# Kernel optimization log

Measured on AMD Instinct MI355X. Metric: run time of the kernel, lower is better.

Reference implementation:

```python
import jax, jax.numpy as jnp
import numpy as np

N = 50000      # num nodes
E = 800000     # num edges (avg degree 16)
F_IN = 64      # num_node_features
D = 64         # layer_hidden_dim (= out_channels per layer)
H = 8          # num_heads
C = D // H     # head_dim = 8
L = 5          # num_gnn_layers


def setup_inputs() -> dict:
    key = jax.random.key(0)
    ks = jax.random.split(key, 8)
    x = jax.random.normal(ks[0], (N, F_IN), jnp.float32)
    edge_index = jax.random.randint(ks[1], (2, E), 0, N, dtype=jnp.int32)
    # input embedding Linear(F_IN, D): weight stored as [in, out]
    W_in = jax.random.normal(ks[2], (F_IN, D), jnp.float32) * 0.1
    b_in = jnp.zeros((D,), jnp.float32)
    # per-layer GAT params, stacked over L layers
    lin_w = jax.random.normal(ks[3], (L, D, D), jnp.float32) * 0.1
    lin_b = jnp.zeros((L, D), jnp.float32)
    att = jax.random.normal(ks[4], (L, H, 2 * C), jnp.float32) * 0.1
    out_bias = jnp.zeros((L, D), jnp.float32)
    ln_g = jnp.ones((L, D), jnp.float32)
    ln_b = jnp.zeros((L, D), jnp.float32)
    return {"x": x, "edge_index": edge_index, "W_in": W_in, "b_in": b_in,
            "lin_w": lin_w, "lin_b": lin_b, "att": att, "out_bias": out_bias,
            "ln_g": ln_g, "ln_b": ln_b}


def _gat_layer(h, src, dst, Wl, bl, al, ob, g, b):
    # h: [N, D] -> per-head features [N, H, C]
    hp = (h @ Wl + bl).reshape(N, H, C)
    xi = hp[dst]          # [E, H, C] target-node features (x_i)
    xj = hp[src]          # [E, H, C] source-node features (x_j)
    # cat([x_i, x_j]) . att  == x_i . att[:, :C] + x_j . att[:, C:]
    alpha = jnp.einsum('ehc,hc->eh', xi, al[:, :C]) + \
            jnp.einsum('ehc,hc->eh', xj, al[:, C:])          # [E, H]
    alpha = jax.nn.leaky_relu(alpha, negative_slope=0.2)
    # segment softmax over target index (numerically stable)
    m = jax.ops.segment_max(alpha, dst, num_segments=N)      # [N, H]
    ea = jnp.exp(alpha - m[dst])
    s = jax.ops.segment_sum(ea, dst, num_segments=N)         # [N, H]
    w = ea / (s[dst] + 1e-16)                                # [E, H]
    # message = x_j * alpha, aggr='add'
    agg = jax.ops.segment_sum(xj * w[:, :, None], dst, num_segments=N)  # [N, H, C]
    out = agg.reshape(N, H * C) + ob
    out = jax.nn.elu(out)
    # LayerNorm over feature dim (eval mode: dropout = identity)
    mu = out.mean(-1, keepdims=True)
    var = out.var(-1, keepdims=True)
    return (out - mu) * jax.lax.rsqrt(var + 1e-5) * g + b


def reference(x, edge_index, W_in, b_in, lin_w, lin_b, att, out_bias, ln_g, ln_b):
    src = edge_index[0]
    dst = edge_index[1]   # PyG source_to_target: index = edge_index[1]
    h = jax.nn.relu(x @ W_in + b_in)
    for l in range(L):
        h = _gat_layer(h, src, dst, lin_w[l], lin_b[l], att[l],
                       out_bias[l], ln_g[l], ln_b[l])
    return h
```

## Files before the change

### kernel.cpp

```cpp
#include <hip/hip_runtime.h>
#include <hip/hip_bf16.h>

#define DD 64
#define LL 5
#define KPAD 64
#define L2E 1.4426950408889634f

typedef __attribute__((ext_vector_type(8))) short short8;
typedef __attribute__((ext_vector_type(4))) float float4v;

__device__ __forceinline__ short f2bf_bits(float f) {
    __hip_bfloat16 h = __float2bfloat16(f);
    return *reinterpret_cast<short*>(&h);
}
__device__ __forceinline__ float bfbits2f(short s) {
    __hip_bfloat16 h = *reinterpret_cast<__hip_bfloat16*>(&s);
    return __bfloat162float(h);
}

__device__ __forceinline__ int sniffw(const unsigned short* xb) {
    int lane = threadIdx.x & 63;
    int e = (xb[lane * 2] >> 7) & 0xFF;
    return __any(e >= 134) ? 1 : 0;
}

__global__ void allcvt_k(const void* __restrict__ x, const void* __restrict__ W_in,
                         const void* __restrict__ b_in, const void* __restrict__ lw,
                         const void* __restrict__ lb, const void* __restrict__ att,
                         const void* __restrict__ ob, const void* __restrict__ lg,
                         const void* __restrict__ lbb,
                         float* __restrict__ wts,
                         unsigned short* __restrict__ whiT, unsigned short* __restrict__ wloT,
                         int* __restrict__ deg, int n) {
    int bid = blockIdx.x;
    int fl = sniffw((const unsigned short*)x);
    if (bid < 104) {
        int i = bid * 256 + threadIdx.x;
        if (i >= 26560) return;
        const void* p; int o;
        if      (i < 4096)  { p = W_in; o = i; }
        else if (i < 4160)  { p = b_in; o = i - 4096; }
        else if (i < 24640) { p = lw;   o = i - 4160; }
        else if (i < 24960) { p = lb;   o = i - 24640; }
        else if (i < 25600) { p = att;  o = i - 24960; }
        else if (i < 25920) { p = ob;   o = i - 25600; }
        else if (i < 26240) { p = lg;   o = i - 25920; }
        else                { p = lbb;  o = i - 26240; }
        wts[i] = fl ? ((const float*)p)[o] : (float)((const __hip_bfloat16*)p)[o];
    } else if (bid < 104 + 96) {
        int i = (bid - 104) * 256 + threadIdx.x;
        if (i >= 6 * 4096) return;
        const void* p; int o;
        if (i < 4096) { p = W_in; o = i; } else { p = lw; o = i - 4096; }
        float v = fl ? ((const float*)p)[o] : (float)((const __hip_bfloat16*)p)[o];
        short hi = f2bf_bits(v);
        short lo = f2bf_bits(v - bfbits2f(hi));
        int mat = i >> 12, rem = i & 4095, k = rem >> 6, col = rem & 63;
        int t = mat * 4096 + col * 64 + k;
        whiT[t] = (unsigned short)hi;
        wloT[t] = (unsigned short)lo;
    } else {
        int i = (bid - 104 - 96) * 256 + threadIdx.x;
        if (i < n) deg[i] = 0;
    }
}

__device__ __forceinline__ void gemm_from_lds(
        const unsigned short (*AH)[72], const unsigned short (*AL)[72],
        const unsigned short* __restrict__ Whi, const unsigned short* __restrict__ Wlo,
        const float* __restrict__ bias, const float* __restrict__ Att,
        unsigned short* __restrict__ hp_out, float* __restrict__ bd,
        float* __restrict__ ss, int base, int n) {
    int lane = threadIdx.x & 63;
    int wave = threadIdx.x >> 6;
    int m = lane & 15;
    int q = lane >> 4;
    int coln = wave * 16 + m;

    short8 ah0 = *reinterpret_cast<const short8*>(&AH[m][q * 8]);
    short8 ah1 = *reinterpret_cast<const short8*>(&AH[m][32 + q * 8]);
    short8 al0 = *reinterpret_cast<const short8*>(&AL[m][q * 8]);
    short8 al1 = *reinterpret_cast<const short8*>(&AL[m][32 + q * 8]);

    short8 bh0 = *reinterpret_cast<const short8*>(Whi + coln * 64 + q * 8);
    short8 bh1 = *reinterpret_cast<const short8*>(Whi + coln * 64 + 32 + q * 8);
    short8 bl0 = *reinterpret_cast<const short8*>(Wlo + coln * 64 + q * 8);
    short8 bl1 = *reinterpret_cast<const short8*>(Wlo + coln * 64 + 32 + q * 8);

    float4v acc = {0.f, 0.f, 0.f, 0.f};
    acc = __builtin_amdgcn_mfma_f32_16x16x32_bf16(ah0, bh0, acc, 0, 0, 0);
    acc = __builtin_amdgcn_mfma_f32_16x16x32_bf16(al0, bh0, acc, 0, 0, 0);
    acc = __builtin_amdgcn_mfma_f32_16x16x32_bf16(ah0, bl0, acc, 0, 0, 0);
    acc = __builtin_amdgcn_mfma_f32_16x16x32_bf16(ah1, bh1, acc, 0, 0, 0);
    acc = __builtin_amdgcn_mfma_f32_16x16x32_bf16(al1, bh1, acc, 0, 0, 0);
    acc = __builtin_amdgcn_mfma_f32_16x16x32_bf16(ah1, bl1, acc, 0, 0, 0);

    float bc = bias[coln];
    int c_ = m & 7;
    int hh = 2 * wave + (m >> 3);
    float attd = Att[hh * 16 + c_];
    float atts = Att[hh * 16 + 8 + c_];
#pragma unroll
    for (int r = 0; r < 4; ++r) {
        int rr = base + q * 4 + r;
        float v = acc[r] + bc;
        short vb = f2bf_bits(v);
        float vr = bfbits2f(vb);
        if (rr < n) hp_out[(size_t)rr * 64 + coln] = (unsigned short)vb;
        float bdv = vr * attd;
        float ssv = vr * atts;
        bdv += __shfl_xor(bdv, 1, 64);
        bdv += __shfl_xor(bdv, 2, 64);
        bdv += __shfl_xor(bdv, 4, 64);
        ssv += __shfl_xor(ssv, 1, 64);
        ssv += __shfl_xor(ssv, 2, 64);
        ssv += __shfl_xor(ssv, 4, 64);
        if ((m & 7) == 0 && rr < n) {
            bd[rr * 8 + hh] = bdv * L2E;
            ss[rr * 8 + hh] = ssv * L2E;
        }
    }
}

__global__ void __launch_bounds__(256) k0c_k(const void* __restrict__ x,
                                             const int* __restrict__ src,
                                             const int* __restrict__ dst,
                                             int* __restrict__ deg,
                                             unsigned short* __restrict__ csr_pad,
                                             const unsigned short* __restrict__ whiT,
                                             const unsigned short* __restrict__ wloT,
                                             const float* __restrict__ bias_in,
                                             const float* __restrict__ bias_l0,
                                             const float* __restrict__ att0,
                                             unsigned short* __restrict__ hp_out,
                                             float* __restrict__ bd, float* __restrict__ ss,
                                             int n, int e, int psize, int chunks, int nbk) {
    __shared__ unsigned short AH[16][72];
    __shared__ unsigned short AL[16][72];
    int bid = blockIdx.x;
    int grp = bid >> 3;
    int sub = bid & 7;

    if ((grp & 1) == 0) {
        int chunk = grp >> 1;
        if (chunk < chunks) {
            int p = sub;
            int lo = p * psize;
            int hi = min(lo + psize, n);
            int ebase = chunk * 2048 + threadIdx.x;
#pragma unroll
            for (int k = 0; k < 8; ++k) {
                int i = ebase + k * 256;
                if (i < e) {
                    int d = dst[i];
                    if (d >= lo && d < hi) {
                        int slot = atomicAdd(&deg[d], 1);
                        if (slot < KPAD) csr_pad[d * KPAD + slot] = (unsigned short)src[i];
                    }
                }
            }
        }
        return;
    }

    int kb = (grp >> 1) * 8 + sub;
    if (kb >= nbk) return;
    int lane = threadIdx.x & 63;
    int wave = threadIdx.x >> 6;
    int m = lane & 15;
    int q = lane >> 4;
    int coln = wave * 16 + m;
    int base = kb * 16;

    int fl = sniffw((const unsigned short*)x);

    {
        int arow = min(base + m, n - 1);
        short8 ah0, ah1, al0, al1;
        if (fl) {
            const float* xr = (const float*)x + (size_t)arow * 64;
            const float4* p0 = reinterpret_cast<const float4*>(xr + q * 8);
            const float4* p1 = reinterpret_cast<const float4*>(xr + 32 + q * 8);
            float4 f00 = p0[0], f01 = p0[1];
            float4 f10 = p1[0], f11 = p1[1];
            float fs0[8] = {f00.x, f00.y, f00.z, f00.w, f01.x, f01.y, f01.z, f01.w};
            float fs1[8] = {f10.x, f10.y, f10.z, f10.w, f11.x, f11.y, f11.z, f11.w};
#pragma unroll
            for (int k = 0; k < 8; ++k) {
                short h0 = f2bf_bits(fs0[k]);
                ah0[k] = h0;
                al0[k] = f2bf_bits(fs0[k] - bfbits2f(h0));
                short h1 = f2bf_bits(fs1[k]);
                ah1[k] = h1;
                al1[k] = f2bf_bits(fs1[k] - bfbits2f(h1));
            }
        } else {
            const unsigned short* xr = (const unsigned short*)x + (size_t)arow * 64;
            ah0 = *reinterpret_cast<const short8*>(xr + q * 8);
            ah1 = *reinterpret_cast<const short8*>(xr + 32 + q * 8);
            short8 z = {0, 0, 0, 0, 0, 0, 0, 0};
            al0 = z;
            al1 = z;
        }
        short8 bh0 = *reinterpret_cast<const short8*>(whiT + coln * 64 + q * 8);
        short8 bh1 = *reinterpret_cast<const short8*>(whiT + coln * 64 + 32 + q * 8);
        short8 bl0 = *reinterpret_cast<const short8*>(wloT + coln * 64 + q * 8);
        short8 bl1 = *reinterpret_cast<const short8*>(wloT + coln * 64 + 32 + q * 8);
        float4v acc = {0.f, 0.f, 0.f, 0.f};
        acc = __builtin_amdgcn_mfma_f32_16x16x32_bf16(ah0, bh0, acc, 0, 0, 0);
        acc = __builtin_amdgcn_mfma_f32_16x16x32_bf16(al0, bh0, acc, 0, 0, 0);
        acc = __builtin_amdgcn_mfma_f32_16x16x32_bf16(ah0, bl0, acc, 0, 0, 0);
        acc = __builtin_amdgcn_mfma_f32_16x16x32_bf16(ah1, bh1, acc, 0, 0, 0);
        acc = __builtin_amdgcn_mfma_f32_16x16x32_bf16(al1, bh1, acc, 0, 0, 0);
        acc = __builtin_amdgcn_mfma_f32_16x16x32_bf16(ah1, bl1, acc, 0, 0, 0);
        float bc = bias_in[coln];
#pragma unroll
        for (int r = 0; r < 4; ++r) {
            float v = fmaxf(acc[r] + bc, 0.f);
            short hi = f2bf_bits(v);
            AH[q * 4 + r][coln] = (unsigned short)hi;
            AL[q * 4 + r][coln] = (unsigned short)f2bf_bits(v - bfbits2f(hi));
        }
    }
    __syncthreads();
    gemm_from_lds(AH, AL, whiT + 4096, wloT + 4096, bias_l0, att0,
                  hp_out, bd, ss, base, n);
}

#define EXJ(W, j) { unsigned ws_ = (e1 & 4) ? ((e1 & 2) ? W.w : W.z) : ((e1 & 2) ? W.y : W.x); \
    j = (e1 & 1) ? (int)(ws_ >> 16) : (int)(ws_ & 0xffffu); j = min(j, nm1); }
#define EXG(W, g0, g1) { unsigned d0_ = (qt & 2) ? W.y : W.x; unsigned d1_ = (qt & 2) ? W.w : W.z; \
    g0 = (qt & 1) ? (int)(d0_ >> 16) : (int)(d0_ & 0xffffu); \
    g1 = (qt & 1) ? (int)(d1_ >> 16) : (int)(d1_ & 0xffffu); \
    g0 = min(g0, nm1); g1 = min(g1, nm1); }
#define FMA4(V, W, A0, A1, A2, A3) \
    A0 = fmaf(__int_as_float((int)(V.x << 16)), W, A0); \
    A1 = fmaf(__int_as_float((int)(V.x & 0xffff0000u)), W, A1); \
    A2 = fmaf(__int_as_float((int)(V.y << 16)), W, A2); \
    A3 = fmaf(__int_as_float((int)(V.y & 0xffff0000u)), W, A3);

#define ISSUE(c, WA, WB) \
    int jA_##c; EXJ(WA, jA_##c) \
    int jB_##c; EXJ(WB, jB_##c) \
    float ssA_##c = ss_in[jA_##c * 8 + h1]; \
    float ssB_##c = ss_in[jB_##c * 8 + h1]; \
    int gA0_##c; int gA1_##c; EXG(WA, gA0_##c, gA1_##c) \
    int gB0_##c; int gB1_##c; EXG(WB, gB0_##c, gB1_##c) \
    uint2 vA0_##c = *reinterpret_cast<const uint2*>(hpbf + (size_t)gA0_##c * 64 + fq4); \
    uint2 vA1_##c = *reinterpret_cast<const uint2*>(hpbf + (size_t)gA1_##c * 64 + fq4); \
    uint2 vB0_##c = *reinterpret_cast<const uint2*>(hpbf + (size_t)gB0_##c * 64 + fq4); \
    uint2 vB1_##c = *reinterpret_cast<const uint2*>(hpbf + (size_t)gB1_##c * 64 + fq4);

#define COMP(c) { \
    int slot_ = c * 8 + e1; \
    if (c < ncA) { \
        float aa_ = bhA + ssA_##c; aa_ = (aa_ > 0.f) ? aa_ : 0.2f * aa_; \
        float wg_ = (slot_ < ddA) ? exp2f(fminf(aa_, 60.f)) : 0.f; \
        sA += wg_; \
        float w0_ = __int_as_float(__builtin_amdgcn_ds_bpermute(bb, __float_as_int(wg_))); \
        float w1_ = __int_as_float(__builtin_amdgcn_ds_bpermute(bb + 128, __float_as_int(wg_))); \
        FMA4(vA0_##c, w0_, aA0, aA1, aA2, aA3) \
        FMA4(vA1_##c, w1_, aA0, aA1, aA2, aA3) \
    } \
    if (c < ncB) { \
        float aa_ = bhB + ssB_##c; aa_ = (aa_ > 0.f) ? aa_ : 0.2f * aa_; \
        float wg_ = (slot_ < ddB) ? exp2f(fminf(aa_, 60.f)) : 0.f; \
        sB += wg_; \
        float w0_ = __int_as_float(__builtin_amdgcn_ds_bpermute(bb, __float_as_int(wg_))); \
        float w1_ = __int_as_float(__builtin_amdgcn_ds_bpermute(bb + 128, __float_as_int(wg_))); \
        FMA4(vB0_##c, w0_, aB0, aB1, aB2, aB3) \
        FMA4(vB1_##c, w1_, aB0, aB1, aB2, aB3) \
    } }

__device__ __forceinline__ void gat_half(
        const unsigned short* __restrict__ hpbf,
        const float* __restrict__ ss_in,
        const unsigned short* __restrict__ csr,
        int uA, int uB, int ddA, int ddB, float bhA, float bhB,
        int e1, int h1, int qt, int fq4, int bb, int nm1,
        int qselA, int qselB,
        float& r0, float& r1, float& r2, float& r3, float& rsum) {
    const uint4* cA = reinterpret_cast<const uint4*>(csr + (size_t)uA * KPAD);
    const uint4* cB = reinterpret_cast<const uint4*>(csr + (size_t)uB * KPAD);
    uint4 wa0 = cA[0], wa1 = cA[1], wa2 = cA[2], wa3 = cA[3];
    uint4 wb0 = cB[0], wb1 = cB[1], wb2 = cB[2], wb3 = cB[3];
    int ncA = (ddA + 7) >> 3;
    int ncB = (ddB + 7) >> 3;
    int ncm = max(ncA, ncB);

    float sA = 0.f, sB = 0.f;
    float aA0 = 0.f, aA1 = 0.f, aA2 = 0.f, aA3 = 0.f;
    float aB0 = 0.f, aB1 = 0.f, aB2 = 0.f, aB3 = 0.f;

    if (ncm <= 2) {
        ISSUE(0, wa0, wb0)
        ISSUE(1, wa1, wb1)
        COMP(0)
        COMP(1)
    } else if (ncm == 3) {
        ISSUE(0, wa0, wb0)
        ISSUE(1, wa1, wb1)
        COMP(0)
        ISSUE(2, wa2, wb2)
        COMP(1)
        COMP(2)
    } else {
        ISSUE(0, wa0, wb0)
        ISSUE(1, wa1, wb1)
        COMP(0)
        ISSUE(2, wa2, wb2)
        COMP(1)
        ISSUE(3, wa3, wb3)
        COMP(2)
        COMP(3)
        for (int c = 4; c < ncm; ++c) {
            uint4 wac = cA[c];
            uint4 wbc = cB[c];
            int jA; EXJ(wac, jA)
            int jB; EXJ(wbc, jB)
            float ssAv = ss_in[jA * 8 + h1];
            float ssBv = ss_in[jB * 8 + h1];
            int gA0; int gA1; EXG(wac, gA0, gA1)
            int gB0; int gB1; EXG(wbc, gB0, gB1)
            uint2 vA0 = *reinterpret_cast<const uint2*>(hpbf + (size_t)gA0 * 64 + fq4);
            uint2 vA1 = *reinterpret_cast<const uint2*>(hpbf + (size_t)gA1 * 64 + fq4);
            uint2 vB0 = *reinterpret_cast<const uint2*>(hpbf + (size_t)gB0 * 64 + fq4);
            uint2 vB1 = *reinterpret_cast<const uint2*>(hpbf + (size_t)gB1 * 64 + fq4);
            int slot_ = c * 8 + e1;
            if (c < ncA) {
                float aa_ = bhA + ssAv; aa_ = (aa_ > 0.f) ? aa_ : 0.2f * aa_;
                float wg_ = (slot_ < ddA) ? exp2f(fminf(aa_, 60.f)) : 0.f;
                sA += wg_;
                float w0_ = __int_as_float(__builtin_amdgcn_ds_bpermute(bb, __float_as_int(wg_)));
                float w1_ = __int_as_float(__builtin_amdgcn_ds_bpermute(bb + 128, __float_as_int(wg_)));
                FMA4(vA0, w0_, aA0, aA1, aA2, aA3)
                FMA4(vA1, w1_, aA0, aA1, aA2, aA3)
            }
            if (c < ncB) {
                float aa_ = bhB + ssBv; aa_ = (aa_ > 0.f) ? aa_ : 0.2f * aa_;
                float wg_ = (slot_ < ddB) ? exp2f(fminf(aa_, 60.f)) : 0.f;
                sB += wg_;
                float w0_ = __int_as_float(__builtin_amdgcn_ds_bpermute(bb, __float_as_int(wg_)));
                float w1_ = __int_as_float(__builtin_amdgcn_ds_bpermute(bb + 128, __float_as_int(wg_)));
                FMA4(vB0, w0_, aB0, aB1, aB2, aB3)
                FMA4(vB1, w1_, aB0, aB1, aB2, aB3)
            }
        }
    }

    float ssumA = sA;
    ssumA += __shfl_xor(ssumA, 8, 64);
    ssumA += __shfl_xor(ssumA, 16, 64);
    ssumA += __shfl_xor(ssumA, 32, 64);
    float ssumB = sB;
    ssumB += __shfl_xor(ssumB, 8, 64);
    ssumB += __shfl_xor(ssumB, 16, 64);
    ssumB += __shfl_xor(ssumB, 32, 64);

    aA0 += __shfl_xor(aA0, 16, 64); aA0 += __shfl_xor(aA0, 32, 64);
    aA1 += __shfl_xor(aA1, 16, 64); aA1 += __shfl_xor(aA1, 32, 64);
    aA2 += __shfl_xor(aA2, 16, 64); aA2 += __shfl_xor(aA2, 32, 64);
    aA3 += __shfl_xor(aA3, 16, 64); aA3 += __shfl_xor(aA3, 32, 64);
    aB0 += __shfl_xor(aB0, 16, 64); aB0 += __shfl_xor(aB0, 32, 64);
    aB1 += __shfl_xor(aB1, 16, 64); aB1 += __shfl_xor(aB1, 32, 64);
    aB2 += __shfl_xor(aB2, 16, 64); aB2 += __shfl_xor(aB2, 32, 64);
    aB3 += __shfl_xor(aB3, 16, 64); aB3 += __shfl_xor(aB3, 32, 64);

    if (qt == qselA) { r0 = aA0; r1 = aA1; r2 = aA2; r3 = aA3; rsum = ssumA; }
    if (qt == qselB) { r0 = aB0; r1 = aB1; r2 = aB2; r3 = aB3; rsum = ssumB; }
}

__global__ void __launch_bounds__(256) layer_k(const unsigned short* __restrict__ hpbf,
                                               const int* __restrict__ deg,
                                               const unsigned short* __restrict__ csr,
                                               const float* __restrict__ bd_in,
                                               const float* __restrict__ ss_in,
                                               const float* __restrict__ ob,
                                               const float* __restrict__ g,
                                               const float* __restrict__ b,
                                               const unsigned short* __restrict__ Wnhi,
                                               const unsigned short* __restrict__ Wnlo,
                                               const float* __restrict__ bias_n,
                                               const float* __restrict__ att_n,
                                               unsigned short* __restrict__ hp_out,
                                               float* __restrict__ bd_out,
                                               float* __restrict__ ss_out,
                                               void* __restrict__ outp,
                                               const unsigned short* __restrict__ xb,
                                               int n, int last) {
    __shared__ unsigned short AH[16][72];
    __shared__ unsigned short AL[16][72];
    int lane = threadIdx.x & 63;
    int wave = threadIdx.x >> 6;
    int base = blockIdx.x * 16;

    int h1 = lane & 7;
    int e1 = lane >> 3;
    int qt = lane >> 4;
    int fq = lane & 15;
    int fq4 = fq * 4;
    int h2 = fq >> 1;
    int bb = qt * 32 + h2 * 4;
    int nm1 = n - 1;

    int fl = last ? sniffw(xb) : 0;

    int nd0 = base + wave * 4;
    int4 dv = *reinterpret_cast<const int4*>(deg + nd0);
    int dd0 = __builtin_amdgcn_readfirstlane((nd0 + 0 < n) ? min(dv.x, KPAD) : 0);
    int dd1 = __builtin_amdgcn_readfirstlane((nd0 + 1 < n) ? min(dv.y, KPAD) : 0);
    int dd2 = __builtin_amdgcn_readfirstlane((nd0 + 2 < n) ? min(dv.z, KPAD) : 0);
    int dd3 = __builtin_amdgcn_readfirstlane((nd0 + 3 < n) ? min(dv.w, KPAD) : 0);
    float bhv0 = bd_in[min(nd0 + 0, nm1) * 8 + h1];
    float bhv1 = bd_in[min(nd0 + 1, nm1) * 8 + h1];
    float bhv2 = bd_in[min(nd0 + 2, nm1) * 8 + h1];
    float bhv3 = bd_in[min(nd0 + 3, nm1) * 8 + h1];
    int u0 = __builtin_amdgcn_readfirstlane(min(nd0 + 0, nm1));
    int u1 = __builtin_amdgcn_readfirstlane(min(nd0 + 1, nm1));
    int u2 = __builtin_amdgcn_readfirstlane(min(nd0 + 2, nm1));
    int u3 = __builtin_amdgcn_readfirstlane(min(nd0 + 3, nm1));

    float r0 = 0.f, r1 = 0.f, r2 = 0.f, r3 = 0.f, rsum = 0.f;

    gat_half(hpbf, ss_in, csr, u0, u1, dd0, dd1, bhv0, bhv1,
             e1, h1, qt, fq4, bb, nm1, 0, 1, r0, r1, r2, r3, rsum);
    gat_half(hpbf, ss_in, csr, u2, u3, dd2, dd3, bhv2, bhv3,
             e1, h1, qt, fq4, bb, nm1, 2, 3, r0, r1, r2, r3, rsum);

    float sh = __int_as_float(
        __builtin_amdgcn_ds_bpermute((qt * 16 + h2) * 4, __float_as_int(rsum)));
    float rinv = __builtin_amdgcn_rcpf(sh + 1e-16f);
    float4 ob4 = ((const float4*)ob)[fq];
    float o0 = r0 * rinv + ob4.x;
    float o1 = r1 * rinv + ob4.y;
    float o2 = r2 * rinv + ob4.z;
    float o3 = r3 * rinv + ob4.w;
    o0 = (o0 > 0.f) ? o0 : exp2f(o0 * L2E) - 1.f;
    o1 = (o1 > 0.f) ? o1 : exp2f(o1 * L2E) - 1.f;
    o2 = (o2 > 0.f) ? o2 : exp2f(o2 * L2E) - 1.f;
    o3 = (o3 > 0.f) ? o3 : exp2f(o3 * L2E) - 1.f;

    float ps = o0 + o1 + o2 + o3;
#pragma unroll
    for (int d = 1; d < 16; d <<= 1) ps += __shfl_xor(ps, d, 64);
    float mu = ps * (1.f / 64.f);
    float d0 = o0 - mu, d1 = o1 - mu, d2v = o2 - mu, d3 = o3 - mu;
    float sq = d0 * d0 + d1 * d1 + d2v * d2v + d3 * d3;
#pragma unroll
    for (int d = 1; d < 16; d <<= 1) sq += __shfl_xor(sq, d, 64);
    float rstd = __builtin_amdgcn_rsqf(sq * (1.f / 64.f) + 1e-5f);
    float4 g4 = ((const float4*)g)[fq];
    float4 b4 = ((const float4*)b)[fq];
    float y0 = d0 * rstd * g4.x + b4.x;
    float y1 = d1 * rstd * g4.y + b4.y;
    float y2 = d2v * rstd * g4.z + b4.z;
    float y3 = d3 * rstd * g4.w + b4.w;

    int onode = nd0 + qt;
    if (!last) {
        int ridx = wave * 4 + qt;
        short hb0 = f2bf_bits(y0), hb1 = f2bf_bits(y1);
        short hb2 = f2bf_bits(y2), hb3 = f2bf_bits(y3);
        unsigned hA = (unsigned short)hb0 | ((unsigned)(unsigned short)hb1 << 16);
        unsigned hB = (unsigned short)hb2 | ((unsigned)(unsigned short)hb3 << 16);
        uint2 yh = {hA, hB};
        unsigned lA = (unsigned short)f2bf_bits(y0 - bfbits2f(hb0)) |
                      ((unsigned)(unsigned short)f2bf_bits(y1 - bfbits2f(hb1)) << 16);
        unsigned lB = (unsigned short)f2bf_bits(y2 - bfbits2f(hb2)) |
                      ((unsigned)(unsigned short)f2bf_bits(y3 - bfbits2f(hb3)) << 16);
        uint2 yl = {lA, lB};
        *reinterpret_cast<uint2*>(&AH[ridx][fq * 4]) = yh;
        *reinterpret_cast<uint2*>(&AL[ridx][fq * 4]) = yl;
    } else if (onode < n) {
        if (fl) {
            float4 y = {y0, y1, y2, y3};
            ((float4*)outp)[(size_t)onode * 16 + fq] = y;
        } else {
            unsigned lo = (unsigned short)f2bf_bits(y0) |
                          ((unsigned)(unsigned short)f2bf_bits(y1) << 16);
            unsigned hi = (unsigned short)f2bf_bits(y2) |
                          ((unsigned)(unsigned short)f2bf_bits(y3) << 16);
            uint2 y = {lo, hi};
            ((uint2*)outp)[(size_t)onode * 16 + fq] = y;
        }
    }

    if (last) return;
    __syncthreads();
    gemm_from_lds(AH, AL, Wnhi, Wnlo, bias_n, att_n, hp_out, bd_out, ss_out, base, n);
}

static void* g_pool = nullptr;
static size_t g_pool_sz = 0;

extern "C" void kernel_launch(void* const* d_in, const int* in_sizes, int n_in,
                              void* d_out, int out_size, void* d_ws, size_t ws_size,
                              hipStream_t stream) {
    const void* x    = d_in[0];
    const int* ei    = (const int*)d_in[1];
    const void* W_in = d_in[2];
    const void* b_in = d_in[3];
    const void* lw   = d_in[4];
    const void* lb   = d_in[5];
    const void* att  = d_in[6];
    const void* ob   = d_in[7];
    const void* lg   = d_in[8];
    const void* lbb  = d_in[9];

    const int n = in_sizes[0] / DD;
    const int e = in_sizes[1] / 2;
    const int* src = ei;
    const int* dst = ei + e;

    auto align256 = [](size_t v) { return (v + 255) & ~(size_t)255; };
    size_t need = 0;
    size_t off_hpA  = need; need += align256((size_t)(n + 32) * DD * 2);
    size_t off_hpB  = need; need += align256((size_t)(n + 32) * DD * 2);
    size_t off_deg  = need; need += align256((size_t)(n + 32) * 4);
    size_t off_csr  = need; need += align256((size_t)n * KPAD * 2);
    size_t off_wts  = need; need += align256((size_t)26560 * 4);
    size_t off_bdA  = need; need += align256((size_t)n * 8 * 4);
    size_t off_ssA  = need; need += align256((size_t)n * 8 * 4);
    size_t off_bdB  = need; need += align256((size_t)n * 8 * 4);
    size_t off_ssB  = need; need += align256((size_t)n * 8 * 4);
    size_t off_whi  = need; need += align256((size_t)6 * 4096 * 2);
    size_t off_wlo  = need; need += align256((size_t)6 * 4096 * 2);

    char* ws;
    if (ws_size >= need) {
        ws = (char*)d_ws;
    } else {
        if (g_pool == nullptr || g_pool_sz < need) {
            hipMalloc(&g_pool, need);
            g_pool_sz = need;
        }
        ws = (char*)g_pool;
    }

    unsigned short* hpA = (unsigned short*)(ws + off_hpA);
    unsigned short* hpB = (unsigned short*)(ws + off_hpB);
    int* deg     = (int*)(ws + off_deg);
    unsigned short* csr = (unsigned short*)(ws + off_csr);
    float* wts   = (float*)(ws + off_wts);
    float* bdA   = (float*)(ws + off_bdA);
    float* ssA   = (float*)(ws + off_ssA);
    float* bdB   = (float*)(ws + off_bdB);
    float* ssB   = (float*)(ws + off_ssB);
    unsigned short* whiT = (unsigned short*)(ws + off_whi);
    unsigned short* wloT = (unsigned short*)(ws + off_wlo);

    float* wb_in = wts + 4096;
    float* wlb   = wts + 24640;
    float* watt  = wts + 24960;
    float* wob   = wts + 25600;
    float* wlg   = wts + 25920;
    float* wlbb  = wts + 26240;

    int degb = (n + 255) / 256;
    allcvt_k<<<104 + 96 + degb, 256, 0, stream>>>(
        x, W_in, b_in, lw, lb, att, ob, lg, lbb,
        wts, whiT, wloT, deg, n);

    int psize = (n + 7) / 8;
    int chunks = (e + 2047) / 2048;
    int nb16 = (n + 15) / 16;
    int k0g = (nb16 + 7) / 8;
    int ngrp = 2 * max(chunks, k0g);
    k0c_k<<<ngrp * 8, 256, 0, stream>>>(
        x, src, dst, deg, csr, whiT, wloT, wb_in, wlb, watt,
        hpA, bdA, ssA, n, e, psize, chunks, nb16);

    for (int l = 0; l < LL; ++l) {
        int last = (l == LL - 1) ? 1 : 0;
        unsigned short* hin = (l & 1) ? hpB : hpA;
        float* bdi = (l & 1) ? bdB : bdA;
        float* ssi = (l & 1) ? ssB : ssA;
        unsigned short* hout = (l & 1) ? hpA : hpB;
        float* bdo = (l & 1) ? bdA : bdB;
        float* sso = (l & 1) ? ssA : ssB;
        layer_k<<<nb16, 256, 0, stream>>>(
            hin, deg, csr, bdi, ssi,
            wob + (size_t)l * DD, wlg + (size_t)l * DD, wlbb + (size_t)l * DD,
            whiT + (size_t)(l + 2) * 4096, wloT + (size_t)(l + 2) * 4096,
            wlb + (size_t)(l + 1) * DD, watt + (size_t)(l + 1) * 128,
            hout, bdo, sso, d_out, (const unsigned short*)x, n, last);
    }
}
```

Before: 268.4 us.

## Fuse CSR build and all GAT layers into one persistent cooperative kernel

```diff
diff --git a/kernel.cpp b/kernel.cpp
--- a/kernel.cpp
+++ b/kernel.cpp
@@ -1,5 +1,8 @@
 #include <hip/hip_runtime.h>
 #include <hip/hip_bf16.h>
+#include <hip/hip_cooperative_groups.h>
+
+namespace cg = cooperative_groups;
 
 #define DD 64
 #define LL 5
@@ -122,57 +125,43 @@
     }
 }
 
-__global__ void __launch_bounds__(256) k0c_k(const void* __restrict__ x,
-                                             const int* __restrict__ src,
-                                             const int* __restrict__ dst,
-                                             int* __restrict__ deg,
-                                             unsigned short* __restrict__ csr_pad,
-                                             const unsigned short* __restrict__ whiT,
-                                             const unsigned short* __restrict__ wloT,
-                                             const float* __restrict__ bias_in,
-                                             const float* __restrict__ bias_l0,
-                                             const float* __restrict__ att0,
-                                             unsigned short* __restrict__ hp_out,
-                                             float* __restrict__ bd, float* __restrict__ ss,
-                                             int n, int e, int psize, int chunks, int nbk) {
-    __shared__ unsigned short AH[16][72];
-    __shared__ unsigned short AL[16][72];
-    int bid = blockIdx.x;
-    int grp = bid >> 3;
-    int sub = bid & 7;
-
-    if ((grp & 1) == 0) {
-        int chunk = grp >> 1;
-        if (chunk < chunks) {
-            int p = sub;
-            int lo = p * psize;
-            int hi = min(lo + psize, n);
-            int ebase = chunk * 2048 + threadIdx.x;
+__device__ __forceinline__ void csr_work(const int* __restrict__ src,
+                                         const int* __restrict__ dst,
+                                         int* __restrict__ deg,
+                                         unsigned short* __restrict__ csr_pad,
+                                         int e, int psize, int n, int chunk, int sub) {
+    int lo = sub * psize;
+    int hi = min(lo + psize, n);
+    int ebase = chunk * 2048 + threadIdx.x;
 #pragma unroll
-            for (int k = 0; k < 8; ++k) {
-                int i = ebase + k * 256;
-                if (i < e) {
-                    int d = dst[i];
-                    if (d >= lo && d < hi) {
-                        int slot = atomicAdd(&deg[d], 1);
-                        if (slot < KPAD) csr_pad[d * KPAD + slot] = (unsigned short)src[i];
-                    }
-                }
+    for (int k = 0; k < 8; ++k) {
+        int i = ebase + k * 256;
+        if (i < e) {
+            int d = dst[i];
+            if (d >= lo && d < hi) {
+                int slot = atomicAdd(&deg[d], 1);
+                if (slot < KPAD) csr_pad[d * KPAD + slot] = (unsigned short)src[i];
             }
         }
-        return;
-    }
-
-    int kb = (grp >> 1) * 8 + sub;
-    if (kb >= nbk) return;
+    }
+}
+
+__device__ __forceinline__ void k0_tile(unsigned short (*AH)[72], unsigned short (*AL)[72],
+                                        const void* __restrict__ x, int fl,
+                                        const unsigned short* __restrict__ whiT,
+                                        const unsigned short* __restrict__ wloT,
+                                        const float* __restrict__ bias_in,
+                                        const float* __restrict__ bias_l0,
+                                        const float* __restrict__ att0,
+                                        unsigned short* __restrict__ hp_out,
+                                        float* __restrict__ bd, float* __restrict__ ss,
+                                        int n, int kb) {
     int lane = threadIdx.x & 63;
     int wave = threadIdx.x >> 6;
     int m = lane & 15;
     int q = lane >> 4;
     int coln = wave * 16 + m;
     int base = kb * 16;
-
-    int fl = sniffw((const unsigned short*)x);
 
     {
         int arow = min(base + m, n - 1);
@@ -370,29 +359,27 @@
     if (qt == qselB) { r0 = aB0; r1 = aB1; r2 = aB2; r3 = aB3; rsum = ssumB; }
 }
 
-__global__ void __launch_bounds__(256) layer_k(const unsigned short* __restrict__ hpbf,
-                                               const int* __restrict__ deg,
-                                               const unsigned short* __restrict__ csr,
-                                               const float* __restrict__ bd_in,
-                                               const float* __restrict__ ss_in,
-                                               const float* __restrict__ ob,
-                                               const float* __restrict__ g,
-                                               const float* __restrict__ b,
-                                               const unsigned short* __restrict__ Wnhi,
-                                               const unsigned short* __restrict__ Wnlo,
-                                               const float* __restrict__ bias_n,
-                                               const float* __restrict__ att_n,
-                                               unsigned short* __restrict__ hp_out,
-                                               float* __restrict__ bd_out,
-                                               float* __restrict__ ss_out,
-                                               void* __restrict__ outp,
-                                               const unsigned short* __restrict__ xb,
-                                               int n, int last) {
-    __shared__ unsigned short AH[16][72];
-    __shared__ unsigned short AL[16][72];
+__device__ __forceinline__ void layer_tile(unsigned short (*AH)[72], unsigned short (*AL)[72],
+                                           const unsigned short* __restrict__ hpbf,
+                                           const int* __restrict__ deg,
+                                           const unsigned short* __restrict__ csr,
+                                           const float* __restrict__ bd_in,
+                                           const float* __restrict__ ss_in,
+                                           const float* __restrict__ ob,
+                                           const float* __restrict__ g,
+                                           const float* __restrict__ b,
+                                           const unsigned short* __restrict__ Wnhi,
+                                           const unsigned short* __restrict__ Wnlo,
+                                           const float* __restrict__ bias_n,
+                                           const float* __restrict__ att_n,
+                                           unsigned short* __restrict__ hp_out,
+                                           float* __restrict__ bd_out,
+                                           float* __restrict__ ss_out,
+                                           void* __restrict__ outp,
+                                           int fl, int n, int last, int tile) {
     int lane = threadIdx.x & 63;
     int wave = threadIdx.x >> 6;
-    int base = blockIdx.x * 16;
+    int base = tile * 16;
 
     int h1 = lane & 7;
     int e1 = lane >> 3;
@@ -402,8 +389,6 @@
     int h2 = fq >> 1;
     int bb = qt * 32 + h2 * 4;
     int nm1 = n - 1;
-
-    int fl = last ? sniffw(xb) : 0;
 
     int nd0 = base + wave * 4;
     int4 dv = *reinterpret_cast<const int4*>(deg + nd0);
@@ -490,8 +475,129 @@
     gemm_from_lds(AH, AL, Wnhi, Wnlo, bias_n, att_n, hp_out, bd_out, ss_out, base, n);
 }
 
+__global__ void __launch_bounds__(256) gnn_k(const void* __restrict__ x,
+                                             const int* __restrict__ src,
+                                             const int* __restrict__ dst,
+                                             int* __restrict__ deg,
+                                             unsigned short* __restrict__ csr,
+                                             const unsigned short* __restrict__ whiT,
+                                             const unsigned short* __restrict__ wloT,
+                                             const float* __restrict__ wts,
+                                             unsigned short* __restrict__ hpA,
+                                             unsigned short* __restrict__ hpB,
+                                             float* __restrict__ bdA, float* __restrict__ ssA,
+                                             float* __restrict__ bdB, float* __restrict__ ssB,
+                                             void* __restrict__ outp,
+                                             int n, int e, int psize, int chunks, int nb16,
+                                             int totA) {
+    __shared__ unsigned short AH[16][72];
+    __shared__ unsigned short AL[16][72];
+    cg::grid_group grid = cg::this_grid();
+    int G = gridDim.x;
+
+    const float* wb_in = wts + 4096;
+    const float* wlb   = wts + 24640;
+    const float* watt  = wts + 24960;
+    const float* wob   = wts + 25600;
+    const float* wlg   = wts + 25920;
+    const float* wlbb  = wts + 26240;
+
+    int fl = sniffw((const unsigned short*)x);
+
+    for (int item = blockIdx.x; item < totA; item += G) {
+        int grp = item >> 3;
+        int sub = item & 7;
+        if ((grp & 1) == 0) {
+            int chunk = grp >> 1;
+            if (chunk < chunks) csr_work(src, dst, deg, csr, e, psize, n, chunk, sub);
+        } else {
+            int kb = (grp >> 1) * 8 + sub;
+            if (kb < nb16) {
+                k0_tile(AH, AL, x, fl, whiT, wloT, wb_in, wlb, watt, hpA, bdA, ssA, n, kb);
+                __syncthreads();
+            }
+        }
+    }
+    grid.sync();
+
+    for (int l = 0; l < LL; ++l) {
+        int last = (l == LL - 1) ? 1 : 0;
+        const unsigned short* hin = (l & 1) ? hpB : hpA;
+        const float* bdi = (l & 1) ? bdB : bdA;
+        const float* ssi = (l & 1) ? ssB : ssA;
+        unsigned short* hout = (l & 1) ? hpA : hpB;
+        float* bdo = (l & 1) ? bdA : bdB;
+        float* sso = (l & 1) ? ssA : ssB;
+        for (int t = blockIdx.x; t < nb16; t += G) {
+            layer_tile(AH, AL, hin, deg, csr, bdi, ssi,
+                       wob + (size_t)l * DD, wlg + (size_t)l * DD, wlbb + (size_t)l * DD,
+                       whiT + (size_t)(l + 2) * 4096, wloT + (size_t)(l + 2) * 4096,
+                       wlb + (size_t)(l + 1) * DD, watt + (size_t)(l + 1) * 128,
+                       hout, bdo, sso, outp, fl, n, last, t);
+            __syncthreads();
+        }
+        if (!last) grid.sync();
+    }
+}
+
+__global__ void __launch_bounds__(256) k0c_k(const void* __restrict__ x,
+                                             const int* __restrict__ src,
+                                             const int* __restrict__ dst,
+                                             int* __restrict__ deg,
+                                             unsigned short* __restrict__ csr_pad,
+                                             const unsigned short* __restrict__ whiT,
+                                             const unsigned short* __restrict__ wloT,
+                                             const float* __restrict__ bias_in,
+                                             const float* __restrict__ bias_l0,
+                                             const float* __restrict__ att0,
+                                             unsigned short* __restrict__ hp_out,
+                                             float* __restrict__ bd, float* __restrict__ ss,
+                                             int n, int e, int psize, int chunks, int nbk) {
+    __shared__ unsigned short AH[16][72];
+    __shared__ unsigned short AL[16][72];
+    int bid = blockIdx.x;
+    int grp = bid >> 3;
+    int sub = bid & 7;
+    if ((grp & 1) == 0) {
+        int chunk = grp >> 1;
+        if (chunk < chunks) csr_work(src, dst, deg, csr_pad, e, psize, n, chunk, sub);
+        return;
+    }
+    int kb = (grp >> 1) * 8 + sub;
+    if (kb >= nbk) return;
+    int fl = sniffw((const unsigned short*)x);
+    k0_tile(AH, AL, x, fl, whiT, wloT, bias_in, bias_l0, att0, hp_out, bd, ss, n, kb);
+}
+
+__global__ void __launch_bounds__(256) layer_k(const unsigned short* __restrict__ hpbf,
+                                               const int* __restrict__ deg,
+                                               const unsigned short* __restrict__ csr,
+                                               const float* __restrict__ bd_in,
+                                               const float* __restrict__ ss_in,
+                                               const float* __restrict__ ob,
+                                               const float* __restrict__ g,
+                                               const float* __restrict__ b,
+                                               const unsigned short* __restrict__ Wnhi,
+                                               const unsigned short* __restrict__ Wnlo,
+                                               const float* __restrict__ bias_n,
+                                               const float* __restrict__ att_n,
+                                               unsigned short* __restrict__ hp_out,
+                                               float* __restrict__ bd_out,
+                                               float* __restrict__ ss_out,
+                                               void* __restrict__ outp,
+                                               const unsigned short* __restrict__ xb,
+                                               int n, int last) {
+    __shared__ unsigned short AH[16][72];
+    __shared__ unsigned short AL[16][72];
+    int fl = last ? sniffw(xb) : 0;
+    layer_tile(AH, AL, hpbf, deg, csr, bd_in, ss_in, ob, g, b, Wnhi, Wnlo,
+               bias_n, att_n, hp_out, bd_out, ss_out, outp, fl, n, last, blockIdx.x);
+}
+
 static void* g_pool = nullptr;
 static size_t g_pool_sz = 0;
+static int g_coop = -1;
+static int g_gridmax = 0;
 
 extern "C" void kernel_launch(void* const* d_in, const int* in_sizes, int n_in,
                               void* d_out, int out_size, void* d_ws, size_t ws_size,
@@ -556,6 +662,19 @@
     float* wlg   = wts + 25920;
     float* wlbb  = wts + 26240;
 
+    if (g_coop < 0) {
+        int dev = 0;
+        hipGetDevice(&dev);
+        int attr = 0;
+        hipDeviceGetAttribute(&attr, hipDeviceAttributeCooperativeLaunch, dev);
+        int occ = 0;
+        hipError_t oe = hipOccupancyMaxActiveBlocksPerMultiprocessor(&occ, gnn_k, 256, 0);
+        hipDeviceProp_t prop;
+        hipGetDeviceProperties(&prop, dev);
+        g_gridmax = (oe == hipSuccess) ? occ * prop.multiProcessorCount : 0;
+        g_coop = (attr != 0 && g_gridmax >= 16) ? 1 : 0;
+    }
+
     int degb = (n + 255) / 256;
     allcvt_k<<<104 + 96 + degb, 256, 0, stream>>>(
         x, W_in, b_in, lw, lb, att, ob, lg, lbb,
@@ -565,8 +684,27 @@
     int chunks = (e + 2047) / 2048;
     int nb16 = (n + 15) / 16;
     int k0g = (nb16 + 7) / 8;
-    int ngrp = 2 * max(chunks, k0g);
-    k0c_k<<<ngrp * 8, 256, 0, stream>>>(
+    int totA = 2 * max(chunks, k0g) * 8;
+
+    if (g_coop) {
+        int G = g_gridmax & ~15;
+        if (G < 16) G = 16;
+        const void* a_x = x; const int* a_src = src; const int* a_dst = dst;
+        int* a_deg = deg; unsigned short* a_csr = csr;
+        const unsigned short* a_whi = whiT; const unsigned short* a_wlo = wloT;
+        const float* a_wts = wts;
+        unsigned short* a_hpA = hpA; unsigned short* a_hpB = hpB;
+        float* a_bdA = bdA; float* a_ssA = ssA; float* a_bdB = bdB; float* a_ssB = ssB;
+        void* a_out = d_out;
+        int a_n = n, a_e = e, a_ps = psize, a_ch = chunks, a_nb = nb16, a_tot = totA;
+        void* args[] = { &a_x, &a_src, &a_dst, &a_deg, &a_csr, &a_whi, &a_wlo, &a_wts,
+                         &a_hpA, &a_hpB, &a_bdA, &a_ssA, &a_bdB, &a_ssB, &a_out,
+                         &a_n, &a_e, &a_ps, &a_ch, &a_nb, &a_tot };
+        hipLaunchCooperativeKernel(gnn_k, dim3(G), dim3(256), args, 0, stream);
+        return;
+    }
+
+    k0c_k<<<totA, 256, 0, stream>>>(
         x, src, dst, deg, csr, whiT, wloT, wb_in, wlb, watt,
         hpA, bdA, ssA, n, e, psize, chunks, nb16);
 
```

Measured after the change: 762.0 us. 2.84x slower.

## Fuse five GAT layer launches into one persistent cooperative kernel with grid sync

Applied to the files above, without the earlier changes.

```diff
diff --git a/kernel.cpp b/kernel.cpp
--- a/kernel.cpp
+++ b/kernel.cpp
@@ -1,5 +1,8 @@
 #include <hip/hip_runtime.h>
 #include <hip/hip_bf16.h>
+#include <hip/hip_cooperative_groups.h>
+
+namespace cg = cooperative_groups;
 
 #define DD 64
 #define LL 5
@@ -370,29 +373,27 @@
     if (qt == qselB) { r0 = aB0; r1 = aB1; r2 = aB2; r3 = aB3; rsum = ssumB; }
 }
 
-__global__ void __launch_bounds__(256) layer_k(const unsigned short* __restrict__ hpbf,
-                                               const int* __restrict__ deg,
-                                               const unsigned short* __restrict__ csr,
-                                               const float* __restrict__ bd_in,
-                                               const float* __restrict__ ss_in,
-                                               const float* __restrict__ ob,
-                                               const float* __restrict__ g,
-                                               const float* __restrict__ b,
-                                               const unsigned short* __restrict__ Wnhi,
-                                               const unsigned short* __restrict__ Wnlo,
-                                               const float* __restrict__ bias_n,
-                                               const float* __restrict__ att_n,
-                                               unsigned short* __restrict__ hp_out,
-                                               float* __restrict__ bd_out,
-                                               float* __restrict__ ss_out,
-                                               void* __restrict__ outp,
-                                               const unsigned short* __restrict__ xb,
-                                               int n, int last) {
-    __shared__ unsigned short AH[16][72];
-    __shared__ unsigned short AL[16][72];
+__device__ __forceinline__ void layer_tile(unsigned short (*AH)[72], unsigned short (*AL)[72],
+                                           const unsigned short* __restrict__ hpbf,
+                                           const int* __restrict__ deg,
+                                           const unsigned short* __restrict__ csr,
+                                           const float* __restrict__ bd_in,
+                                           const float* __restrict__ ss_in,
+                                           const float* __restrict__ ob,
+                                           const float* __restrict__ g,
+                                           const float* __restrict__ b,
+                                           const unsigned short* __restrict__ Wnhi,
+                                           const unsigned short* __restrict__ Wnlo,
+                                           const float* __restrict__ bias_n,
+                                           const float* __restrict__ att_n,
+                                           unsigned short* __restrict__ hp_out,
+                                           float* __restrict__ bd_out,
+                                           float* __restrict__ ss_out,
+                                           void* __restrict__ outp,
+                                           int fl, int n, int last, int tile) {
     int lane = threadIdx.x & 63;
     int wave = threadIdx.x >> 6;
-    int base = blockIdx.x * 16;
+    int base = tile * 16;
 
     int h1 = lane & 7;
     int e1 = lane >> 3;
@@ -402,8 +403,6 @@
     int h2 = fq >> 1;
     int bb = qt * 32 + h2 * 4;
     int nm1 = n - 1;
-
-    int fl = last ? sniffw(xb) : 0;
 
     int nd0 = base + wave * 4;
     int4 dv = *reinterpret_cast<const int4*>(deg + nd0);
@@ -490,8 +489,77 @@
     gemm_from_lds(AH, AL, Wnhi, Wnlo, bias_n, att_n, hp_out, bd_out, ss_out, base, n);
 }
 
+__global__ void __launch_bounds__(256, 4) layers5_k(
+        const int* __restrict__ deg, const unsigned short* __restrict__ csr,
+        const unsigned short* __restrict__ whiT, const unsigned short* __restrict__ wloT,
+        const float* __restrict__ wts,
+        unsigned short* __restrict__ hpA, unsigned short* __restrict__ hpB,
+        float* __restrict__ bdA, float* __restrict__ ssA,
+        float* __restrict__ bdB, float* __restrict__ ssB,
+        void* __restrict__ outp, const unsigned short* __restrict__ xb,
+        int n, int nb16) {
+    __shared__ unsigned short AH[16][72];
+    __shared__ unsigned short AL[16][72];
+    cg::grid_group grid = cg::this_grid();
+    int G = gridDim.x;
+
+    const float* wlb  = wts + 24640;
+    const float* watt = wts + 24960;
+    const float* wob  = wts + 25600;
+    const float* wlg  = wts + 25920;
+    const float* wlbb = wts + 26240;
+
+    int fl = sniffw(xb);
+
+    for (int l = 0; l < LL; ++l) {
+        int last = (l == LL - 1) ? 1 : 0;
+        const unsigned short* hin = (l & 1) ? hpB : hpA;
+        const float* bdi = (l & 1) ? bdB : bdA;
+        const float* ssi = (l & 1) ? ssB : ssA;
+        unsigned short* hout = (l & 1) ? hpA : hpB;
+        float* bdo = (l & 1) ? bdA : bdB;
+        float* sso = (l & 1) ? ssA : ssB;
+        for (int t = blockIdx.x; t < nb16; t += G) {
+            layer_tile(AH, AL, hin, deg, csr, bdi, ssi,
+                       wob + (size_t)l * DD, wlg + (size_t)l * DD, wlbb + (size_t)l * DD,
+                       whiT + (size_t)(l + 2) * 4096, wloT + (size_t)(l + 2) * 4096,
+                       wlb + (size_t)(l + 1) * DD, watt + (size_t)(l + 1) * 128,
+                       hout, bdo, sso, outp, fl, n, last, t);
+            __syncthreads();
+        }
+        if (!last) grid.sync();
+    }
+}
+
+__global__ void __launch_bounds__(256) layer_k(const unsigned short* __restrict__ hpbf,
+                                               const int* __restrict__ deg,
+                                               const unsigned short* __restrict__ csr,
+                                               const float* __restrict__ bd_in,
+                                               const float* __restrict__ ss_in,
+                                               const float* __restrict__ ob,
+                                               const float* __restrict__ g,
+                                               const float* __restrict__ b,
+                                               const unsigned short* __restrict__ Wnhi,
+                                               const unsigned short* __restrict__ Wnlo,
+                                               const float* __restrict__ bias_n,
+                                               const float* __restrict__ att_n,
+                                               unsigned short* __restrict__ hp_out,
+                                               float* __restrict__ bd_out,
+                                               float* __restrict__ ss_out,
+                                               void* __restrict__ outp,
+                                               const unsigned short* __restrict__ xb,
+                                               int n, int last) {
+    __shared__ unsigned short AH[16][72];
+    __shared__ unsigned short AL[16][72];
+    int fl = last ? sniffw(xb) : 0;
+    layer_tile(AH, AL, hpbf, deg, csr, bd_in, ss_in, ob, g, b, Wnhi, Wnlo,
+               bias_n, att_n, hp_out, bd_out, ss_out, outp, fl, n, last, blockIdx.x);
+}
+
 static void* g_pool = nullptr;
 static size_t g_pool_sz = 0;
+static int g_coop = -1;
+static int g_gridL = 0;
 
 extern "C" void kernel_launch(void* const* d_in, const int* in_sizes, int n_in,
                               void* d_out, int out_size, void* d_ws, size_t ws_size,
@@ -556,6 +624,19 @@
     float* wlg   = wts + 25920;
     float* wlbb  = wts + 26240;
 
+    if (g_coop < 0) {
+        int dev = 0;
+        hipGetDevice(&dev);
+        int attr = 0;
+        hipDeviceGetAttribute(&attr, hipDeviceAttributeCooperativeLaunch, dev);
+        int occ = 0;
+        hipError_t oe = hipOccupancyMaxActiveBlocksPerMultiprocessor(&occ, layers5_k, 256, 0);
+        hipDeviceProp_t prop;
+        hipGetDeviceProperties(&prop, dev);
+        g_gridL = (oe == hipSuccess) ? occ * prop.multiProcessorCount : 0;
+        g_coop = (attr != 0 && g_gridL >= 64) ? 1 : 0;
+    }
+
     int degb = (n + 255) / 256;
     allcvt_k<<<104 + 96 + degb, 256, 0, stream>>>(
         x, W_in, b_in, lw, lb, att, ob, lg, lbb,
@@ -569,6 +650,23 @@
     k0c_k<<<ngrp * 8, 256, 0, stream>>>(
         x, src, dst, deg, csr, whiT, wloT, wb_in, wlb, watt,
         hpA, bdA, ssA, n, e, psize, chunks, nb16);
+
+    if (g_coop) {
+        int G = min(g_gridL, nb16);
+        const int* a_deg = deg; const unsigned short* a_csr = csr;
+        const unsigned short* a_whi = whiT; const unsigned short* a_wlo = wloT;
+        const float* a_wts = wts;
+        unsigned short* a_hpA = hpA; unsigned short* a_hpB = hpB;
+        float* a_bdA = bdA; float* a_ssA = ssA; float* a_bdB = bdB; float* a_ssB = ssB;
+        void* a_out = d_out;
+        const unsigned short* a_xb = (const unsigned short*)x;
+        int a_n = n, a_nb = nb16;
+        void* args[] = { &a_deg, &a_csr, &a_whi, &a_wlo, &a_wts,
+                         &a_hpA, &a_hpB, &a_bdA, &a_ssA, &a_bdB, &a_ssB,
+                         &a_out, &a_xb, &a_n, &a_nb };
+        hipLaunchCooperativeKernel(layers5_k, dim3(G), dim3(256), args, 0, stream);
+        return;
+    }
 
     for (int l = 0; l < LL; ++l) {
         int last = (l == LL - 1) ? 1 : 0;
```

New measurement: 617.4 us. 130% more time.
